# Kernel optimization log

Hardware: AMD Instinct MI355X
Metric: run time of the kernel (lower is better)

The kernel has to match this reference:

```python
import jax, jax.numpy as jnp
import numpy as np
from jax import lax

STRIDES = [4, 8, 16, 32, 64]
SIZES = [32.0, 64.0, 128.0, 256.0, 512.0]
RATIOS = [0.5, 1.0, 2.0]
IMG_H = IMG_W = 1024.0
NMS_T = 0.7
PRE = 1000      # PRE_NMS_TOPK_TEST
POST = 1000     # POST_NMS_TOPK_TEST
MIN_SIZE = 0.0
N = 2
FEAT = [(256, 256), (128, 128), (64, 64), (32, 32), (16, 16)]
SCALE_CLAMP = float(np.log(1000.0 / 16.0))


def make_anchors(H, W, stride, size):
    # detectron2 DefaultAnchorGenerator: area=size^2, w=sqrt(area/r), h=w*r; grid offsets = stride*arange
    r = np.array(RATIOS)
    ws = np.sqrt(size * size / r)
    hs = ws * r
    base = np.stack([-ws / 2, -hs / 2, ws / 2, hs / 2], axis=1)  # [A,4]
    sx = np.arange(W) * stride
    sy = np.arange(H) * stride
    yy, xx = np.meshgrid(sy, sx, indexing='ij')
    shifts = np.stack([xx, yy, xx, yy], axis=-1).reshape(-1, 1, 4)  # [H*W,1,4]
    return jnp.asarray((shifts + base[None]).reshape(-1, 4), jnp.float32)  # [H*W*A,4]


def conv2d(x, w, b, pad):
    y = lax.conv_general_dilated(x, w, (1, 1), [(pad, pad), (pad, pad)],
                                 dimension_numbers=('NCHW', 'OIHW', 'NCHW'))
    return y + b[None, :, None, None]


def apply_deltas(deltas, anchors):
    # Box2BoxTransform.apply_deltas with weights (1,1,1,1)
    w = anchors[..., 2] - anchors[..., 0]
    h = anchors[..., 3] - anchors[..., 1]
    cx = anchors[..., 0] + 0.5 * w
    cy = anchors[..., 1] + 0.5 * h
    dx, dy, dw, dh = deltas[..., 0], deltas[..., 1], deltas[..., 2], deltas[..., 3]
    dw = jnp.minimum(dw, SCALE_CLAMP)
    dh = jnp.minimum(dh, SCALE_CLAMP)
    pcx = dx * w + cx
    pcy = dy * h + cy
    pw = jnp.exp(dw) * w
    ph = jnp.exp(dh) * h
    return jnp.stack([pcx - 0.5 * pw, pcy - 0.5 * ph, pcx + 0.5 * pw, pcy + 0.5 * ph], axis=-1)


def pairwise_iou(b):
    area = (b[:, 2] - b[:, 0]) * (b[:, 3] - b[:, 1])
    lt = jnp.maximum(b[:, None, :2], b[None, :, :2])
    rb = jnp.minimum(b[:, None, 2:], b[None, :, 2:])
    wh = jnp.clip(rb - lt, 0.0)
    inter = wh[..., 0] * wh[..., 1]
    return inter / jnp.maximum(area[:, None] + area[None, :] - inter, 1e-9)


def nms_keep(boxes, valid):
    # boxes already sorted by score desc; sequential greedy NMS keep mask
    K = boxes.shape[0]
    M = pairwise_iou(boxes)
    idx = jnp.arange(K)

    def body(i, keep):
        sup = (M[i] > NMS_T) & (idx > i) & keep[i]
        return keep & (~sup)

    return lax.fori_loop(0, K, body, valid)


def rpn_forward(feats, conv_w, conv_b, obj_w, obj_b, delta_w, delta_b):
    all_boxes, all_scores = [], []
    lim = jnp.array([IMG_W, IMG_H, IMG_W, IMG_H], jnp.float32)
    for x, (H, W), stride, size in zip(feats, FEAT, STRIDES, SIZES):
        t = jax.nn.relu(conv2d(x, conv_w, conv_b, 1))
        logits = conv2d(t, obj_w, obj_b, 0)      # [N,A,H,W]
        deltas = conv2d(t, delta_w, delta_b, 0)  # [N,4A,H,W]
        A = logits.shape[1]
        logits = logits.transpose(0, 2, 3, 1).reshape(N, -1)                       # [N,H*W*A]
        deltas = deltas.reshape(N, A, 4, H, W).transpose(0, 3, 4, 1, 2).reshape(N, -1, 4)
        anchors = make_anchors(H, W, stride, size)
        props = apply_deltas(deltas, anchors[None])                                # [N,H*W*A,4]
        k = min(PRE, props.shape[1])
        scores, idx = lax.top_k(logits, k)                                         # [N,k]
        boxes = jnp.take_along_axis(props, idx[..., None], axis=1)                 # [N,k,4]
        boxes = jnp.clip(boxes, 0.0, lim)                                          # clip to image
        valid = ((boxes[..., 2] - boxes[..., 0]) > MIN_SIZE) & ((boxes[..., 3] - boxes[..., 1]) > MIN_SIZE)
        keep = lax.stop_gradient(jax.vmap(nms_keep)(boxes, valid))                 # NMS is no_grad in torch
        all_boxes.append(boxes)
        all_scores.append(jnp.where(keep, scores, -1e9))
    boxes = jnp.concatenate(all_boxes, axis=1)
    scores = jnp.concatenate(all_scores, axis=1)
    fs, fi = lax.top_k(scores, POST)                                               # final sort-by-score
    fb = jnp.take_along_axis(boxes, fi[..., None], axis=1)
    return fb, fs


def setup_inputs() -> dict:
    key = jax.random.key(0)
    ks = jax.random.split(key, 8)
    d = {}
    for i, (name, (H, W)) in enumerate(zip(['p2', 'p3', 'p4', 'p5', 'p6'], FEAT)):
        d[name] = jax.random.normal(ks[i], (N, 256, H, W), jnp.float32)
    d['conv_w'] = jax.random.normal(ks[5], (256, 256, 3, 3), jnp.float32) * 0.01
    d['conv_b'] = jnp.zeros((256,), jnp.float32)
    d['obj_w'] = jax.random.normal(ks[6], (3, 256, 1, 1), jnp.float32) * 0.01
    d['obj_b'] = jnp.zeros((3,), jnp.float32)
    d['delta_w'] = jax.random.normal(ks[7], (12, 256, 1, 1), jnp.float32) * 0.01
    d['delta_b'] = jnp.zeros((12,), jnp.float32)
    return d


def reference(p2, p3, p4, p5, p6, conv_w, conv_b, obj_w, obj_b, delta_w, delta_b):
    return rpn_forward([p2, p3, p4, p5, p6], conv_w, conv_b, obj_w, obj_b, delta_w, delta_b)
```

## Files before the change

kernel.cpp:

```cpp
#include <hip/hip_runtime.h>
#include <stdint.h>

#define DEVI __device__ __forceinline__

#define S_TOT 261888
#define NIMG  2
#define SCLD  4.135166556742356

__constant__ int    c_S[5]    = {196608, 49152, 12288, 3072, 768};
__constant__ int    c_loff[5] = {0, 196608, 245760, 258048, 261120};
__constant__ int    c_K[5]    = {1000, 1000, 1000, 1000, 768};
__constant__ int    c_Wl[5]   = {256, 128, 64, 32, 16};
__constant__ int    c_str[5]  = {4, 8, 16, 32, 64};
__constant__ double c_sz[5]   = {32.0, 64.0, 128.0, 256.0, 512.0};
__constant__ double c_rat[3]  = {0.5, 1.0, 2.0};
__constant__ int    c_boff[6] = {0, 256, 320, 336, 340, 341};
__constant__ int    c_Hl[5]   = {256, 128, 64, 32, 16};

DEVI unsigned key_of(float f) {
  unsigned u = __float_as_uint(f);
  return (u & 0x80000000u) ? ~u : (u | 0x80000000u);
}
DEVI float key_dec(unsigned k) {
  unsigned u = (k & 0x80000000u) ? (k & 0x7fffffffu) : ~k;
  return __uint_as_float(u);
}

__global__ void transpose_w(const float* __restrict__ w, float* __restrict__ wT4) {
  int k  = blockIdx.x;
  int co = threadIdx.x;
  int ci = k / 9, j = k - ci * 9;
  int chunk = ci >> 3, cc = ci & 7;
  int g = co >> 4, i = co & 15;
  wT4[(size_t)chunk * 18432 + cc * 2304 + g * 144 + j * 16 + i] = w[co * 2304 + k];
}

__global__ __launch_bounds__(1024, 4) void conv_fused(
    const float* __restrict__ x0, const float* __restrict__ x1,
    const float* __restrict__ x2, const float* __restrict__ x3,
    const float* __restrict__ x4,
    const float* __restrict__ wT4,
    const float* __restrict__ cb, const float* __restrict__ ow,
    const float* __restrict__ ob, const float* __restrict__ dwt,
    const float* __restrict__ db, float* __restrict__ logits,
    float* __restrict__ deltas)
{
  __shared__ float lds[21024];
  float* const wlds = lds + 2592;
  const int tid = threadIdx.x;
  const int n = blockIdx.y;
  const int b = blockIdx.x;
  int l = 0;
#pragma unroll
  for (int q = 1; q < 5; ++q) if (b >= c_boff[q]) l = q;
  const int t = b - c_boff[l];
  const int H = c_Hl[l], W = H;
  const int tilesx = 16 >> l;
  const int tx = t & (tilesx - 1), ty = t >> (4 - l);
  const int px0 = tx << 4, py0 = ty << 4;
  const int loff = c_loff[l];
  const float* xin = (l == 0) ? x0 : (l == 1) ? x1 : (l == 2) ? x2 : (l == 3) ? x3 : x4;
  xin += (size_t)n * 256 * H * W;

  const int lane = tid & 63, wv = tid >> 6;
  const int px = lane & 15, p = lane >> 4;

  float acc[64];
#pragma unroll
  for (int i = 0; i < 64; ++i) acc[i] = 0.f;

  for (int ch = 0; ch < 32; ++ch) {
    const int ci0 = ch << 3;
    __syncthreads();
    for (int tt = tid; tt < 2592; tt += 1024) {
      int ci = tt / 324, rem = tt - ci * 324;
      int ry = rem / 18, rx = rem - ry * 18;
      int gy = py0 + ry - 1, gx = px0 + rx - 1;
      float v = 0.f;
      if (gy >= 0 && gy < H && gx >= 0 && gx < W)
        v = xin[((size_t)(ci0 + ci) * H + gy) * W + gx];
      lds[tt] = v;
    }
    {
      const float4* wg = (const float4*)(wT4 + (size_t)ch * 18432);
      float4* wl = (float4*)wlds;
      for (int tt = tid; tt < 4608; tt += 1024) wl[tt] = wg[tt];
    }
    __syncthreads();
#pragma unroll 1
    for (int cc = 0; cc < 8; ++cc) {
      const float* wr = wlds + cc * 2304 + wv * 144;
      const int pb = cc * 324 + p * 18 + px;
#pragma unroll 1
      for (int ky = 0; ky < 3; ++ky) {
        const int rb = pb + ky * 18;
        float q0[3], q1[3], q2[3], q3[3];
#pragma unroll
        for (int c = 0; c < 3; ++c) {
          q0[c] = lds[rb + c];
          q1[c] = lds[rb + 72 + c];
          q2[c] = lds[rb + 144 + c];
          q3[c] = lds[rb + 216 + c];
        }
        const float* wk = wr + ky * 48;
#pragma unroll
        for (int kx = 0; kx < 3; ++kx) {
          const float* wt = wk + kx * 16;
          const float4 wa = *(const float4*)(wt + 0);
          const float4 wb = *(const float4*)(wt + 4);
          const float4 wc = *(const float4*)(wt + 8);
          const float4 wd = *(const float4*)(wt + 12);
          const float v0 = q0[kx], v1 = q1[kx], v2 = q2[kx], v3 = q3[kx];
          acc[ 0] = fmaf(wa.x, v0, acc[ 0]); acc[ 1] = fmaf(wa.y, v0, acc[ 1]);
          acc[ 2] = fmaf(wa.z, v0, acc[ 2]); acc[ 3] = fmaf(wa.w, v0, acc[ 3]);
          acc[ 4] = fmaf(wb.x, v0, acc[ 4]); acc[ 5] = fmaf(wb.y, v0, acc[ 5]);
          acc[ 6] = fmaf(wb.z, v0, acc[ 6]); acc[ 7] = fmaf(wb.w, v0, acc[ 7]);
          acc[ 8] = fmaf(wc.x, v0, acc[ 8]); acc[ 9] = fmaf(wc.y, v0, acc[ 9]);
          acc[10] = fmaf(wc.z, v0, acc[10]); acc[11] = fmaf(wc.w, v0, acc[11]);
          acc[12] = fmaf(wd.x, v0, acc[12]); acc[13] = fmaf(wd.y, v0, acc[13]);
          acc[14] = fmaf(wd.z, v0, acc[14]); acc[15] = fmaf(wd.w, v0, acc[15]);
          acc[16] = fmaf(wa.x, v1, acc[16]); acc[17] = fmaf(wa.y, v1, acc[17]);
          acc[18] = fmaf(wa.z, v1, acc[18]); acc[19] = fmaf(wa.w, v1, acc[19]);
          acc[20] = fmaf(wb.x, v1, acc[20]); acc[21] = fmaf(wb.y, v1, acc[21]);
          acc[22] = fmaf(wb.z, v1, acc[22]); acc[23] = fmaf(wb.w, v1, acc[23]);
          acc[24] = fmaf(wc.x, v1, acc[24]); acc[25] = fmaf(wc.y, v1, acc[25]);
          acc[26] = fmaf(wc.z, v1, acc[26]); acc[27] = fmaf(wc.w, v1, acc[27]);
          acc[28] = fmaf(wd.x, v1, acc[28]); acc[29] = fmaf(wd.y, v1, acc[29]);
          acc[30] = fmaf(wd.z, v1, acc[30]); acc[31] = fmaf(wd.w, v1, acc[31]);
          acc[32] = fmaf(wa.x, v2, acc[32]); acc[33] = fmaf(wa.y, v2, acc[33]);
          acc[34] = fmaf(wa.z, v2, acc[34]); acc[35] = fmaf(wa.w, v2, acc[35]);
          acc[36] = fmaf(wb.x, v2, acc[36]); acc[37] = fmaf(wb.y, v2, acc[37]);
          acc[38] = fmaf(wb.z, v2, acc[38]); acc[39] = fmaf(wb.w, v2, acc[39]);
          acc[40] = fmaf(wc.x, v2, acc[40]); acc[41] = fmaf(wc.y, v2, acc[41]);
          acc[42] = fmaf(wc.z, v2, acc[42]); acc[43] = fmaf(wc.w, v2, acc[43]);
          acc[44] = fmaf(wd.x, v2, acc[44]); acc[45] = fmaf(wd.y, v2, acc[45]);
          acc[46] = fmaf(wd.z, v2, acc[46]); acc[47] = fmaf(wd.w, v2, acc[47]);
          acc[48] = fmaf(wa.x, v3, acc[48]); acc[49] = fmaf(wa.y, v3, acc[49]);
          acc[50] = fmaf(wa.z, v3, acc[50]); acc[51] = fmaf(wa.w, v3, acc[51]);
          acc[52] = fmaf(wb.x, v3, acc[52]); acc[53] = fmaf(wb.y, v3, acc[53]);
          acc[54] = fmaf(wb.z, v3, acc[54]); acc[55] = fmaf(wb.w, v3, acc[55]);
          acc[56] = fmaf(wc.x, v3, acc[56]); acc[57] = fmaf(wc.y, v3, acc[57]);
          acc[58] = fmaf(wc.z, v3, acc[58]); acc[59] = fmaf(wc.w, v3, acc[59]);
          acc[60] = fmaf(wd.x, v3, acc[60]); acc[61] = fmaf(wd.y, v3, acc[61]);
          acc[62] = fmaf(wd.z, v3, acc[62]); acc[63] = fmaf(wd.w, v3, acc[63]);
        }
      }
    }
  }

  const int co0 = __builtin_amdgcn_readfirstlane(wv << 4);
#pragma unroll
  for (int h = 0; h < 4; ++h) {
    float part[15];
#pragma unroll
    for (int f = 0; f < 15; ++f) part[f] = 0.f;
#pragma unroll
    for (int i = 0; i < 16; ++i) {
      float tv = fmaxf(acc[h * 16 + i] + cb[co0 + i], 0.f);
#pragma unroll
      for (int f = 0; f < 3; ++f)  part[f]     = fmaf(tv, ow[f * 256 + co0 + i],  part[f]);
#pragma unroll
      for (int f = 0; f < 12; ++f) part[3 + f] = fmaf(tv, dwt[f * 256 + co0 + i], part[3 + f]);
    }
    __syncthreads();
#pragma unroll
    for (int f = 0; f < 15; ++f) lds[wv * 960 + f * 64 + lane] = part[f];
    __syncthreads();
    for (int tt = tid; tt < 960; tt += 1024) {
      float s = 0.f;
#pragma unroll
      for (int w2 = 0; w2 < 16; ++w2) s += lds[w2 * 960 + tt];
      int f = tt >> 6, pp = tt & 63;
      int gx = px0 + (pp & 15), gy = py0 + (pp >> 4) + 4 * h;
      int cell = gy * W + gx;
      if (f < 3) {
        logits[(size_t)n * S_TOT + loff + cell * 3 + f] = s + ob[f];
      } else {
        int chn = f - 3, a = chn >> 2, c = chn & 3;
        deltas[(((size_t)n * S_TOT + loff + cell * 3 + a) << 2) + c] = s + db[chn];
      }
    }
  }
}

__global__ __launch_bounds__(1024) void topk_kernel(
    const float* __restrict__ logits, const float* __restrict__ deltas,
    float* __restrict__ selscore, float* __restrict__ selbox,
    unsigned* __restrict__ selvalid)
{
  const int tid = threadIdx.x;
  const int nl = blockIdx.x, n = nl / 5, l = nl % 5;
  const int Sl = c_S[l], loff = c_loff[l], Kl = c_K[l], Wl = c_Wl[l], strl = c_str[l];
  const float* sc = logits + (size_t)n * S_TOT + loff;

  __shared__ unsigned hist[256];
  __shared__ unsigned sh_prefix, sh_need, s_base, s_cb;
  __shared__ unsigned waveTot[16], waveOff[16];
  __shared__ unsigned long long sortbuf[1024];

  unsigned prefix = 0, need = (unsigned)Kl;
  for (int p = 0; p < 4; ++p) {
    for (int i = tid; i < 256; i += 1024) hist[i] = 0;
    __syncthreads();
    const int shift = 24 - p * 8;
    for (int i = tid; i < Sl; i += 1024) {
      unsigned k = key_of(sc[i]);
      if (p == 0 || (k >> (shift + 8)) == prefix)
        atomicAdd(&hist[(k >> shift) & 255u], 1u);
    }
    __syncthreads();
    if (tid == 0) {
      unsigned cum = 0;
      for (int b = 255; b >= 0; --b) {
        unsigned c = hist[b];
        if (cum + c >= need) { sh_prefix = (prefix << 8) | (unsigned)b; sh_need = need - cum; break; }
        cum += c;
      }
    }
    __syncthreads();
    prefix = sh_prefix; need = sh_need;
    __syncthreads();
  }
  const unsigned Tkey = prefix;

  if (tid == 0) s_base = 0;
  __syncthreads();
  for (int pass = 0; pass < 2; ++pass) {
    for (int st = 0; st < Sl; st += 1024) {
      const int i = st + tid;
      bool flag = false; unsigned k = 0;
      if (i < Sl) {
        k = key_of(sc[i]);
        flag = (pass == 0) ? (k > Tkey) : (k == Tkey);
      }
      unsigned long long m = __ballot(flag);
      const int lane = tid & 63, w = tid >> 6;
      unsigned mypre = (unsigned)__popcll(m & ((1ull << lane) - 1ull));
      if (lane == 0) waveTot[w] = (unsigned)__popcll(m);
      __syncthreads();
      if (tid == 0) {
        unsigned ss = 0;
        for (int q = 0; q < 16; ++q) { waveOff[q] = ss; ss += waveTot[q]; }
        s_cb = s_base; s_base += ss;
      }
      __syncthreads();
      if (flag) {
        unsigned pos = s_cb + waveOff[w] + mypre;
        if (pos < (unsigned)Kl)
          sortbuf[pos] = (((unsigned long long)k) << 32) |
                         (unsigned long long)(0xFFFFFFFFu - (unsigned)i);
      }
      __syncthreads();
    }
  }
  if (tid >= Kl) sortbuf[tid] = (unsigned long long)(0xFFFFFFFFu - (unsigned)tid);
  __syncthreads();

  for (int k2 = 2; k2 <= 1024; k2 <<= 1) {
    for (int j = k2 >> 1; j > 0; j >>= 1) {
      const int i = tid, ixj = i ^ j;
      if (ixj > i) {
        unsigned long long a = sortbuf[i], b = sortbuf[ixj];
        const bool desc = (i & k2) == 0;
        if (desc ? (a < b) : (a > b)) { sortbuf[i] = b; sortbuf[ixj] = a; }
      }
      __syncthreads();
    }
  }

  const int r = tid;
  const int o = nl * 1024 + r;
  if (r < Kl) {
    unsigned long long v = sortbuf[r];
    unsigned k = (unsigned)(v >> 32);
    unsigned ai = 0xFFFFFFFFu - (unsigned)(v & 0xFFFFFFFFull);
    float score = key_dec(k);
    int cell = (int)(ai / 3u), a = (int)(ai % 3u);
    int xg = cell % Wl, yg = cell / Wl;
    double rr = c_rat[a], sz = c_sz[l];
    double wsd = sqrt(sz * sz / rr);
    double hw = 0.5 * wsd, hh = 0.5 * wsd * rr;
    double xs = (double)(xg * strl), ys = (double)(yg * strl);
    float a0 = (float)(xs - hw), a1 = (float)(ys - hh);
    float a2 = (float)(xs + hw), a3 = (float)(ys + hh);
    const float* dp = deltas + (((size_t)n * S_TOT + loff + ai) << 2);
    float dx = dp[0], dy = dp[1], dw_ = dp[2], dh_ = dp[3];
    float aw = a2 - a0, ah = a3 - a1;
    float cx = a0 + 0.5f * aw, cy = a1 + 0.5f * ah;
    dw_ = fminf(dw_, (float)SCLD); dh_ = fminf(dh_, (float)SCLD);
    float pcx = dx * aw + cx, pcy = dy * ah + cy;
    float pw = expf(dw_) * aw, ph = expf(dh_) * ah;
    float b0 = fminf(fmaxf(pcx - 0.5f * pw, 0.f), 1024.f);
    float b1 = fminf(fmaxf(pcy - 0.5f * ph, 0.f), 1024.f);
    float b2 = fminf(fmaxf(pcx + 0.5f * pw, 0.f), 1024.f);
    float b3 = fminf(fmaxf(pcy + 0.5f * ph, 0.f), 1024.f);
    unsigned valid = ((b2 - b0) > 0.f && (b3 - b1) > 0.f) ? 1u : 0u;
    selscore[o] = score;
    selbox[o * 4 + 0] = b0; selbox[o * 4 + 1] = b1;
    selbox[o * 4 + 2] = b2; selbox[o * 4 + 3] = b3;
    selvalid[o] = valid;
  } else {
    selscore[o] = -1e9f;
    selbox[o * 4 + 0] = 0.f; selbox[o * 4 + 1] = 0.f;
    selbox[o * 4 + 2] = 0.f; selbox[o * 4 + 3] = 0.f;
    selvalid[o] = 0u;
  }
}

__global__ __launch_bounds__(256) void nms_sup(
    const float* __restrict__ selbox, unsigned long long* __restrict__ sup)
{
  int gid = blockIdx.x * 256 + threadIdx.x;
  int w = gid & 15, i = (gid >> 4) & 1023, nl = gid >> 14;
  if (nl >= 10) return;
  int l = nl % 5, Kl = c_K[l];
  unsigned long long bits = 0;
  if (i < Kl) {
    const float* bi = selbox + (size_t)(nl * 1024 + i) * 4;
    float x0 = bi[0], y0 = bi[1], x1 = bi[2], y1 = bi[3];
    float ar = (x1 - x0) * (y1 - y0);
    int jlo = w * 64; if (jlo < i + 1) jlo = i + 1;
    int jhi = w * 64 + 64; if (jhi > Kl) jhi = Kl;
    for (int j = jlo; j < jhi; ++j) {
      const float* bj = selbox + (size_t)(nl * 1024 + j) * 4;
      float u0 = fmaxf(x0, bj[0]), v0 = fmaxf(y0, bj[1]);
      float u1 = fminf(x1, bj[2]), v1 = fminf(y1, bj[3]);
      float iw = fmaxf(u1 - u0, 0.f), ih = fmaxf(v1 - v0, 0.f);
      float inter = iw * ih;
      float aj = (bj[2] - bj[0]) * (bj[3] - bj[1]);
      float iou = inter / fmaxf(ar + aj - inter, 1e-9f);
      if (iou > 0.7f) bits |= 1ull << (j - w * 64);
    }
  }
  sup[(size_t)(nl * 1024 + i) * 16 + w] = bits;
}

__global__ __launch_bounds__(64) void nms_reduce(
    const unsigned* __restrict__ selvalid, const unsigned long long* __restrict__ sup,
    const float* __restrict__ selscore, float* __restrict__ scnms)
{
  const int nl = blockIdx.x, tid = threadIdx.x;
  const int l = nl % 5, Kl = c_K[l];
  unsigned long long keep = 0;
  if (tid < 16) {
    for (int t = 0; t < 64; ++t) {
      int r = tid * 64 + t;
      if (r < Kl && selvalid[nl * 1024 + r]) keep |= 1ull << t;
    }
  }
  const unsigned long long* srow = sup + (size_t)nl * 1024 * 16;
  unsigned long long rowA = (tid < 16) ? srow[(size_t)0 * 16 + tid] : 0;
  unsigned long long rowB = (tid < 16 && Kl > 1) ? srow[(size_t)1 * 16 + tid] : 0;
  for (int i = 0; i < Kl; i += 2) {
    unsigned long long kw = __shfl(keep, i >> 6);
    unsigned long long cur = rowA;
    rowA = (tid < 16 && i + 2 < Kl) ? srow[(size_t)(i + 2) * 16 + tid] : 0;
    if (((kw >> (i & 63)) & 1ull) && tid < 16) keep &= ~cur;
    kw = __shfl(keep, (i + 1) >> 6);
    cur = rowB;
    rowB = (tid < 16 && i + 3 < Kl) ? srow[(size_t)(i + 3) * 16 + tid] : 0;
    if (((kw >> ((i + 1) & 63)) & 1ull) && tid < 16) keep &= ~cur;
  }
  for (int r = tid; r < 1024; r += 64) {
    unsigned long long wv = __shfl(keep, r >> 6);
    bool kp = (r < Kl) && ((wv >> (r & 63)) & 1ull);
    scnms[nl * 1024 + r] = kp ? selscore[nl * 1024 + r] : -1e9f;
  }
}

DEVI float cand_score(const float* scnms, int n, int g) {
  int l = g / 1000;
  int r = g - l * 1000;
  return scnms[((n * 5 + l) << 10) + r];
}

__global__ __launch_bounds__(1024) void final_topk(
    const float* __restrict__ scnms, const float* __restrict__ selbox,
    float* __restrict__ out)
{
  const int tid = threadIdx.x;
  const int n = blockIdx.x;
  const int S = 4768;

  __shared__ unsigned hist[256];
  __shared__ unsigned sh_prefix, sh_need, s_base, s_cb;
  __shared__ unsigned waveTot[16], waveOff[16];
  __shared__ unsigned long long sortbuf[1024];

  unsigned prefix = 0, need = 1000;
  for (int p = 0; p < 4; ++p) {
    for (int i = tid; i < 256; i += 1024) hist[i] = 0;
    __syncthreads();
    const int shift = 24 - p * 8;
    for (int i = tid; i < S; i += 1024) {
      unsigned k = key_of(cand_score(scnms, n, i));
      if (p == 0 || (k >> (shift + 8)) == prefix)
        atomicAdd(&hist[(k >> shift) & 255u], 1u);
    }
    __syncthreads();
    if (tid == 0) {
      unsigned cum = 0;
      for (int b = 255; b >= 0; --b) {
        unsigned c = hist[b];
        if (cum + c >= need) { sh_prefix = (prefix << 8) | (unsigned)b; sh_need = need - cum; break; }
        cum += c;
      }
    }
    __syncthreads();
    prefix = sh_prefix; need = sh_need;
    __syncthreads();
  }
  const unsigned Tkey = prefix;

  if (tid == 0) s_base = 0;
  __syncthreads();
  for (int pass = 0; pass < 2; ++pass) {
    for (int st = 0; st < S; st += 1024) {
      const int i = st + tid;
      bool flag = false; unsigned k = 0;
      if (i < S) {
        k = key_of(cand_score(scnms, n, i));
        flag = (pass == 0) ? (k > Tkey) : (k == Tkey);
      }
      unsigned long long m = __ballot(flag);
      const int lane = tid & 63, w = tid >> 6;
      unsigned mypre = (unsigned)__popcll(m & ((1ull << lane) - 1ull));
      if (lane == 0) waveTot[w] = (unsigned)__popcll(m);
      __syncthreads();
      if (tid == 0) {
        unsigned ss = 0;
        for (int q = 0; q < 16; ++q) { waveOff[q] = ss; ss += waveTot[q]; }
        s_cb = s_base; s_base += ss;
      }
      __syncthreads();
      if (flag) {
        unsigned pos = s_cb + waveOff[w] + mypre;
        if (pos < 1000u)
          sortbuf[pos] = (((unsigned long long)k) << 32) |
                         (unsigned long long)(0xFFFFFFFFu - (unsigned)i);
      }
      __syncthreads();
    }
  }
  if (tid >= 1000) sortbuf[tid] = (unsigned long long)(0xFFFFFFFFu - (unsigned)tid);
  __syncthreads();

  for (int k2 = 2; k2 <= 1024; k2 <<= 1) {
    for (int j = k2 >> 1; j > 0; j >>= 1) {
      const int i = tid, ixj = i ^ j;
      if (ixj > i) {
        unsigned long long a = sortbuf[i], b = sortbuf[ixj];
        const bool desc = (i & k2) == 0;
        if (desc ? (a < b) : (a > b)) { sortbuf[i] = b; sortbuf[ixj] = a; }
      }
      __syncthreads();
    }
  }

  if (tid < 1000) {
    unsigned long long v = sortbuf[tid];
    unsigned k = (unsigned)(v >> 32);
    int g = (int)(0xFFFFFFFFu - (unsigned)(v & 0xFFFFFFFFull));
    int l = g / 1000, r = g - l * 1000;
    const float* b = selbox + ((size_t)((n * 5 + l) * 1024 + r)) * 4;
    size_t ob_ = ((size_t)n * 1000 + tid) * 4;
    out[ob_ + 0] = b[0]; out[ob_ + 1] = b[1];
    out[ob_ + 2] = b[2]; out[ob_ + 3] = b[3];
    out[8000 + n * 1000 + tid] = key_dec(k);
  }
}

extern "C" void kernel_launch(void* const* d_in, const int* in_sizes, int n_in,
                              void* d_out, int out_size, void* d_ws, size_t ws_size,
                              hipStream_t stream)
{
  const float* feats[5];
  for (int i = 0; i < 5; ++i) feats[i] = (const float*)d_in[i];
  const float* conv_w  = (const float*)d_in[5];
  const float* conv_b  = (const float*)d_in[6];
  const float* obj_w   = (const float*)d_in[7];
  const float* obj_b   = (const float*)d_in[8];
  const float* delta_w = (const float*)d_in[9];
  const float* delta_b = (const float*)d_in[10];

  char* wsp = (char*)d_ws;
  float* wT4      = (float*)wsp;  wsp += (size_t)2304 * 256 * 4;
  float* logits   = (float*)wsp;  wsp += (size_t)NIMG * S_TOT * 4;
  float* deltas   = (float*)wsp;  wsp += (size_t)NIMG * S_TOT * 16;
  float* selscore = (float*)wsp;  wsp += (size_t)10 * 1024 * 4;
  float* selbox   = (float*)wsp;  wsp += (size_t)10 * 1024 * 16;
  unsigned* selvalid = (unsigned*)wsp; wsp += (size_t)10 * 1024 * 4;
  float* scnms    = (float*)wsp;  wsp += (size_t)10 * 1024 * 4;
  unsigned long long* sup = (unsigned long long*)wsp;
  wsp += (size_t)10 * 1024 * 16 * 8;

  transpose_w<<<dim3(2304), dim3(256), 0, stream>>>(conv_w, wT4);

  conv_fused<<<dim3(341, NIMG), dim3(1024), 0, stream>>>(
      feats[0], feats[1], feats[2], feats[3], feats[4],
      wT4, conv_b, obj_w, obj_b, delta_w, delta_b, logits, deltas);

  topk_kernel<<<dim3(10), dim3(1024), 0, stream>>>(logits, deltas,
                                                   selscore, selbox, selvalid);
  nms_sup<<<dim3(640), dim3(256), 0, stream>>>(selbox, sup);
  nms_reduce<<<dim3(10), dim3(64), 0, stream>>>(selvalid, sup, selscore, scnms);
  final_topk<<<dim3(NIMG), dim3(1024), 0, stream>>>(scnms, selbox, (float*)d_out);
}
```

Before: 3.370 ms.

## Transpose conv input tile in LDS and load pixel columns with vector reads

Stores the haloed input tile column-major (x-major, padded rows of 20) and changes the pixel-to-thread mapping so each thread handles four consecutive rows per column. The 18 scalar LDS reads per ky iteration are replaced by three float4+float2 column loads per channel, with the ky loop fully unrolled. The output row mapping in the epilogue is adjusted to match. This aims to cut LDS instruction count in the inner loop, at the cost of more LDS space, strided scatter writes when filling the tile, and more registers held live.

```diff
diff --git a/kernel.cpp b/kernel.cpp
--- a/kernel.cpp
+++ b/kernel.cpp
@@ -45,8 +45,8 @@
     const float* __restrict__ db, float* __restrict__ logits,
     float* __restrict__ deltas)
 {
-  __shared__ float lds[21024];
-  float* const wlds = lds + 2592;
+  __shared__ float lds[21312];
+  float* const wlds = lds + 2880;
   const int tid = threadIdx.x;
   const int n = blockIdx.y;
   const int b = blockIdx.x;
@@ -79,7 +79,7 @@
       float v = 0.f;
       if (gy >= 0 && gy < H && gx >= 0 && gx < W)
         v = xin[((size_t)(ci0 + ci) * H + gy) * W + gx];
-      lds[tt] = v;
+      lds[ci * 360 + rx * 20 + ry] = v;
     }
     {
       const float4* wg = (const float4*)(wT4 + (size_t)ch * 18432);
@@ -90,27 +90,27 @@
 #pragma unroll 1
     for (int cc = 0; cc < 8; ++cc) {
       const float* wr = wlds + cc * 2304 + wv * 144;
-      const int pb = cc * 324 + p * 18 + px;
-#pragma unroll 1
+      const int pb = cc * 360 + px * 20 + (p << 2);
+      float c0[6], c1[6], c2[6];
+      *(float4*)&c0[0] = *(const float4*)&lds[pb +  0];
+      *(float2*)&c0[4] = *(const float2*)&lds[pb +  4];
+      *(float4*)&c1[0] = *(const float4*)&lds[pb + 20];
+      *(float2*)&c1[4] = *(const float2*)&lds[pb + 24];
+      *(float4*)&c2[0] = *(const float4*)&lds[pb + 40];
+      *(float2*)&c2[4] = *(const float2*)&lds[pb + 44];
+#pragma unroll
       for (int ky = 0; ky < 3; ++ky) {
-        const int rb = pb + ky * 18;
-        float q0[3], q1[3], q2[3], q3[3];
-#pragma unroll
-        for (int c = 0; c < 3; ++c) {
-          q0[c] = lds[rb + c];
-          q1[c] = lds[rb + 72 + c];
-          q2[c] = lds[rb + 144 + c];
-          q3[c] = lds[rb + 216 + c];
-        }
-        const float* wk = wr + ky * 48;
 #pragma unroll
         for (int kx = 0; kx < 3; ++kx) {
-          const float* wt = wk + kx * 16;
+          const float* wt = wr + (ky * 3 + kx) * 16;
           const float4 wa = *(const float4*)(wt + 0);
           const float4 wb = *(const float4*)(wt + 4);
           const float4 wc = *(const float4*)(wt + 8);
           const float4 wd = *(const float4*)(wt + 12);
-          const float v0 = q0[kx], v1 = q1[kx], v2 = q2[kx], v3 = q3[kx];
+          const float v0 = (kx == 0) ? c0[ky + 0] : (kx == 1) ? c1[ky + 0] : c2[ky + 0];
+          const float v1 = (kx == 0) ? c0[ky + 1] : (kx == 1) ? c1[ky + 1] : c2[ky + 1];
+          const float v2 = (kx == 0) ? c0[ky + 2] : (kx == 1) ? c1[ky + 2] : c2[ky + 2];
+          const float v3 = (kx == 0) ? c0[ky + 3] : (kx == 1) ? c1[ky + 3] : c2[ky + 3];
           acc[ 0] = fmaf(wa.x, v0, acc[ 0]); acc[ 1] = fmaf(wa.y, v0, acc[ 1]);
           acc[ 2] = fmaf(wa.z, v0, acc[ 2]); acc[ 3] = fmaf(wa.w, v0, acc[ 3]);
           acc[ 4] = fmaf(wb.x, v0, acc[ 4]); acc[ 5] = fmaf(wb.y, v0, acc[ 5]);
@@ -171,7 +171,7 @@
 #pragma unroll
       for (int w2 = 0; w2 < 16; ++w2) s += lds[w2 * 960 + tt];
       int f = tt >> 6, pp = tt & 63;
-      int gx = px0 + (pp & 15), gy = py0 + (pp >> 4) + 4 * h;
+      int gx = px0 + (pp & 15), gy = py0 + ((pp >> 4) << 2) + h;
       int cell = gy * W + gx;
       if (f < 3) {
         logits[(size_t)n * S_TOT + loff + cell * 3 + f] = s + ob[f];
```

Result: faster. 3.166 ms (-6.1%).
